# Optimization experiments

Measured on AMD Instinct MI355X. Metric: run time of the kernel, lower is better.

## Reference

```python
import jax, jax.numpy as jnp
import numpy as np

N = 50000    # total nodes in a batched graph
E = 200000   # directed edges (before self loops)
G = 256      # molecules per batch
F_IN = 64    # atom features
H = 4        # gat heads
CH = 128     # hidden_channels (per head)
D = H * CH   # 512, concat width
MLP_H = 128  # hidden_channels * mlp_hidden_factor
NEG_SLOPE = 0.2


def _gat(x, src, dst, W, a_src, a_dst, b, concat):
    """PyG GATConv (eval mode, self loops already added to src/dst)."""
    n = x.shape[0]
    heads, ch = a_src.shape
    h = (x @ W).reshape(n, heads, ch)                       # [N,H,C]
    e = jax.nn.leaky_relu((h * a_src).sum(-1)[src]
                          + (h * a_dst).sum(-1)[dst], NEG_SLOPE)  # [E,H]
    emax = jax.ops.segment_max(e, dst, num_segments=n)
    emax = jnp.where(jnp.isfinite(emax), emax, 0.0)
    p = jnp.exp(e - emax[dst])
    denom = jax.ops.segment_sum(p, dst, num_segments=n)
    alpha = p / (denom[dst] + 1e-16)                        # segment softmax over dst
    out = jax.ops.segment_sum(h[src] * alpha[..., None], dst, num_segments=n)
    out = out.reshape(n, heads * ch) if concat else out.mean(axis=1)
    return out + b


def _encoder(x, edge_index, batch, p):
    n = x.shape[0]
    loop = jnp.arange(n, dtype=edge_index.dtype)            # GATConv add_self_loops=True
    src = jnp.concatenate([edge_index[0], loop])
    dst = jnp.concatenate([edge_index[1], loop])
    x = jax.nn.elu(_gat(x, src, dst, p['W1'], p['as1'], p['ad1'], p['b1'], True))
    x = jax.nn.elu(_gat(x, src, dst, p['W2'], p['as2'], p['ad2'], p['b2'], True))
    x = _gat(x, src, dst, p['W3'], p['as3'], p['ad3'], p['b3'], False)
    emb = jax.ops.segment_max(x, batch, num_segments=G)     # global_max_pool
    return jnp.where(jnp.isfinite(emb), emb, 0.0)


def setup_inputs() -> dict:
    key = jax.random.key(0)
    ks = jax.random.split(key, 24)
    rn = lambda k, s, sc=0.1: jax.random.normal(k, s, jnp.float32) * sc
    return dict(
        x1=rn(ks[0], (N, F_IN), 1.0),
        edge_index1=jax.random.randint(ks[1], (2, E), 0, N, dtype=jnp.int32),
        batch1=jnp.sort(jax.random.randint(ks[2], (N,), 0, G, dtype=jnp.int32)),
        x2=rn(ks[3], (N, F_IN), 1.0),
        edge_index2=jax.random.randint(ks[4], (2, E), 0, N, dtype=jnp.int32),
        batch2=jnp.sort(jax.random.randint(ks[5], (N,), 0, G, dtype=jnp.int32)),
        W1=rn(ks[6], (F_IN, D)), as1=rn(ks[7], (H, CH)), ad1=rn(ks[8], (H, CH)),
        b1=jnp.zeros((D,), jnp.float32),
        W2=rn(ks[9], (D, D)), as2=rn(ks[10], (H, CH)), ad2=rn(ks[11], (H, CH)),
        b2=jnp.zeros((D,), jnp.float32),
        W3=rn(ks[12], (D, CH)), as3=rn(ks[13], (1, CH)), ad3=rn(ks[14], (1, CH)),
        b3=jnp.zeros((CH,), jnp.float32),
        mw1=rn(ks[15], (2 * CH, MLP_H)), mb1=jnp.zeros((MLP_H,), jnp.float32),
        mw2=rn(ks[16], (MLP_H, 1)), mb2=jnp.zeros((1,), jnp.float32),
    )


def reference(x1, edge_index1, batch1, x2, edge_index2, batch2,
              W1, as1, ad1, b1, W2, as2, ad2, b2, W3, as3, ad3, b3,
              mw1, mb1, mw2, mb2):
    p = dict(W1=W1, as1=as1, ad1=ad1, b1=b1,
             W2=W2, as2=as2, ad2=ad2, b2=b2,
             W3=W3, as3=as3, ad3=ad3, b3=b3)
    e1 = _encoder(x1, edge_index1, batch1, p)               # [G, CH]
    e2 = _encoder(x2, edge_index2, batch2, p)               # [G, CH]
    z = jnp.concatenate([e1, e2], axis=-1)                  # [G, 2*CH]
    return jax.nn.relu(z @ mw1 + mb1) @ mw2 + mb2           # [G, 1]
```

## Files before the change

kernel.cpp:

```cpp
#include <hip/hip_runtime.h>
#include <cstdint>

namespace {
constexpr int kN = 50000;
constexpr int kE = 200000;
constexpr int kE2 = kE + kN;
constexpr int kG = 256;
constexpr float kNegSlope = 0.2f;
}

using half8   = __attribute__((ext_vector_type(8))) _Float16;
using floatx4 = __attribute__((ext_vector_type(4))) float;

__device__ __forceinline__ void gld_lds16(const void* g, void* l) {
  __builtin_amdgcn_global_load_lds(
      (const __attribute__((address_space(1))) unsigned int*)g,
      (__attribute__((address_space(3))) unsigned int*)l, 16, 0, 0);
}

__device__ __forceinline__ float fexp(float x) {
  return __builtin_amdgcn_exp2f(x * 1.44269504088896f);
}

template <int OUTF16, int BN, int CT>
__global__ __launch_bounds__(512, 2) void gemm_ring(
    const _Float16* __restrict__ A, const _Float16* __restrict__ B,
    void* __restrict__ Cv, int M, int N, int K) {
  constexpr int ASL = 1024;
  constexpr int BSL = BN * 4;
  constexpr int SLOT = (ASL + BSL) * 16;
  constexpr int LPT = (ASL + BSL) / 512;
  constexpr int WN = (BN == 256) ? 4 : 2;
  constexpr int WM = 8 / WN;
  constexpr int WTM = 256 / WM;
  constexpr int WTN = BN / WN;
  constexpr int MI = WTM / 16;
  constexpr int NI = WTN / 16;
  __shared__ alignas(16) char smem[4 * SLOT];
  const int t = threadIdx.x;
  const int w = t >> 6, l = t & 63;
  const int x = blockIdx.x & 7, s = blockIdx.x >> 3;
  const int col = (CT == 1) ? 0 : (s & (CT - 1));
  const int rt = ((CT == 1) ? s : (s >> 1)) * 8 + x;
  const int bm = rt * 256;
  const int bn = col * BN;
  if (bm >= M) return;
  const int wr = w / WN, wc = w % WN;
  const int quad = l >> 4, lrow = l & 15;

  floatx4 acc[MI][NI];
#pragma unroll
  for (int mi = 0; mi < MI; ++mi)
#pragma unroll
    for (int ni = 0; ni < NI; ++ni) acc[mi][ni] = (floatx4){0.f, 0.f, 0.f, 0.f};

  auto stageA = [&](int kt) {
    char* buf = smem + (size_t)(kt & 3) * SLOT;
    int k0 = kt * 32;
    k0 = (k0 > K - 32) ? (K - 32) : k0;
#pragma unroll
    for (int i = 0; i < 2; ++i) {
      const int sl = i * 512 + t;
      const int row = ((sl >> 6) << 4) + (sl & 15);
      const int q = (sl >> 4) & 3;
      int ga = bm + row;
      ga = (ga < M) ? ga : (M - 1);
      gld_lds16(A + (size_t)ga * K + k0 + q * 8, buf + sl * 16);
    }
  };
  auto stageB = [&](int kt) {
    char* buf = smem + (size_t)(kt & 3) * SLOT + ASL * 16;
    int k0 = kt * 32;
    k0 = (k0 > K - 32) ? (K - 32) : k0;
#pragma unroll
    for (int i = 0; i < LPT - 2; ++i) {
      const int sl = i * 512 + t;
      const int row = ((sl >> 6) << 4) + (sl & 15);
      const int q = (sl >> 4) & 3;
      gld_lds16(B + (size_t)(bn + row) * K + k0 + q * 8, buf + sl * 16);
    }
  };

  stageA(0); stageB(0);
  stageA(1); stageB(1);
  stageA(2); stageB(2);

  const int NT = K >> 5;
  for (int kt = 0; kt < NT; ++kt) {
    char* bufc = smem + (size_t)(kt & 3) * SLOT;
    stageA(kt + 3);
    if constexpr (BN == 256)
      asm volatile("s_waitcnt vmcnt(10)" ::: "memory");
    else
      asm volatile("s_waitcnt vmcnt(8)" ::: "memory");
    __builtin_amdgcn_s_barrier();
    asm volatile("" ::: "memory");
    half8 fa[MI], fb[NI];
#pragma unroll
    for (int ni = 0; ni < NI; ++ni)
      fb[ni] = *(const half8*)(bufc + ASL * 16 + ((wc * NI + ni) << 10) + l * 16);
#pragma unroll
    for (int mi = 0; mi < MI / 2; ++mi)
      fa[mi] = *(const half8*)(bufc + ((wr * MI + mi) << 10) + l * 16);
    __builtin_amdgcn_s_setprio(1);
#pragma unroll
    for (int mi = 0; mi < MI / 2; ++mi)
#pragma unroll
      for (int ni = 0; ni < NI; ++ni)
        acc[mi][ni] = __builtin_amdgcn_mfma_f32_16x16x32_f16(
            fa[mi], fb[ni], acc[mi][ni], 0, 0, 0);
    __builtin_amdgcn_s_setprio(0);
    stageB(kt + 3);
#pragma unroll
    for (int mi = MI / 2; mi < MI; ++mi)
      fa[mi] = *(const half8*)(bufc + ((wr * MI + mi) << 10) + l * 16);
    __builtin_amdgcn_s_setprio(1);
#pragma unroll
    for (int mi = MI / 2; mi < MI; ++mi)
#pragma unroll
      for (int ni = 0; ni < NI; ++ni)
        acc[mi][ni] = __builtin_amdgcn_mfma_f32_16x16x32_f16(
            fa[mi], fb[ni], acc[mi][ni], 0, 0, 0);
    __builtin_amdgcn_s_setprio(0);
    asm volatile("" ::: "memory");
    __builtin_amdgcn_s_barrier();
  }
  asm volatile("s_waitcnt vmcnt(0)" ::: "memory");
  const int colbase = bn + wc * WTN + lrow;
#pragma unroll
  for (int mi = 0; mi < MI; ++mi) {
    const int rbase = bm + wr * WTM + mi * 16 + quad * 4;
#pragma unroll
    for (int r = 0; r < 4; ++r) {
      const int grow = rbase + r;
      if (grow < M) {
        if constexpr (OUTF16) {
          _Float16* C = (_Float16*)Cv;
#pragma unroll
          for (int ni = 0; ni < NI; ++ni)
            C[(size_t)grow * N + colbase + ni * 16] = (_Float16)acc[mi][ni][r];
        } else {
          float* C = (float*)Cv;
#pragma unroll
          for (int ni = 0; ni < NI; ++ni)
            C[(size_t)grow * N + colbase + ni * 16] = acc[mi][ni][r];
        }
      }
    }
  }
}

__global__ void wt_split_all(const float* __restrict__ W1, _Float16* Th1,
                             const float* __restrict__ W2, _Float16* Th2,
                             const float* __restrict__ W3, _Float16* Th3) {
  int idx = blockIdx.x * blockDim.x + threadIdx.x;
  const float* W;
  _Float16* Th;
  int K, N;
  if (idx < 64 * 512) {
    W = W1; Th = Th1; K = 64; N = 512;
  } else if (idx < 64 * 512 + 512 * 512) {
    idx -= 64 * 512;
    W = W2; Th = Th2; K = 512; N = 512;
  } else if (idx < 64 * 512 + 512 * 512 + 512 * 128) {
    idx -= 64 * 512 + 512 * 512;
    W = W3; Th = Th3; K = 512; N = 128;
  } else {
    return;
  }
  const int k = idx / N;
  const int n = idx - k * N;
  Th[n * K + k] = (_Float16)W[idx];
}

__global__ void prep2(const float* __restrict__ x0, const float* __restrict__ x1,
                      _Float16* __restrict__ Xh, int* __restrict__ cnt,
                      int* __restrict__ total) {
  const int idx = blockIdx.x * blockDim.x + threadIdx.x;
  const int half = kN * 64;
  if (idx < half) Xh[idx] = (_Float16)x0[idx];
  else if (idx < 2 * half) Xh[idx] = (_Float16)x1[idx - half];
  if (idx < 2 * kN) cnt[idx] = 1;
  if (idx == 0) *total = 0;
}
__global__ void prep(const float* __restrict__ X, _Float16* __restrict__ Xh,
                     int* __restrict__ cnt, int* __restrict__ total, int nsplit,
                     int n) {
  const int idx = blockIdx.x * blockDim.x + threadIdx.x;
  if (idx < nsplit) Xh[idx] = (_Float16)X[idx];
  if (idx < n) cnt[idx] = 1;
  if (idx == 0) *total = 0;
}

__global__ void count_edges2(const int* __restrict__ d0, const int* __restrict__ d1,
                             int* __restrict__ cnt) {
  const int i = blockIdx.x * blockDim.x + threadIdx.x;
  if (i < kE) atomicAdd(&cnt[d0[i]], 1);
  else if (i < 2 * kE) atomicAdd(&cnt[d1[i - kE] + kN], 1);
}
__global__ void fill_edges2(const int* __restrict__ s0, const int* __restrict__ d0,
                            const int* __restrict__ s1, const int* __restrict__ d1,
                            int* __restrict__ cursor, int* __restrict__ csr) {
  const int i = blockIdx.x * blockDim.x + threadIdx.x;
  if (i < kE) {
    const int p = atomicAdd(&cursor[d0[i]], 1);
    csr[p] = s0[i];
  } else if (i < 2 * kE) {
    const int j = i - kE;
    const int p = atomicAdd(&cursor[d1[j] + kN], 1);
    csr[p] = s1[j] + kN;
  }
}
__global__ void count_edges(const int* __restrict__ dst, int* __restrict__ cnt,
                            int ne) {
  const int i = blockIdx.x * blockDim.x + threadIdx.x;
  if (i < ne) atomicAdd(&cnt[dst[i]], 1);
}
__global__ void fill_edges(const int* __restrict__ src, const int* __restrict__ dst,
                           int* __restrict__ cursor, int* __restrict__ csr, int ne) {
  const int i = blockIdx.x * blockDim.x + threadIdx.x;
  if (i < ne) {
    const int p = atomicAdd(&cursor[dst[i]], 1);
    csr[p] = src[i];
  }
}
__global__ void alloc_ranges(const int* __restrict__ cnt, int* __restrict__ start,
                             int* __restrict__ cursor, int* __restrict__ total,
                             int* __restrict__ csr, int n) {
  const int i = blockIdx.x * blockDim.x + threadIdx.x;
  const int lane = threadIdx.x & 63;
  const int v = (i < n) ? cnt[i] : 0;
  int sc = v;
#pragma unroll
  for (int off = 1; off < 64; off <<= 1) {
    const int t = __shfl_up(sc, off);
    if (lane >= off) sc += t;
  }
  const int wtot = __shfl(sc, 63);
  int base = 0;
  if (lane == 63) base = atomicAdd(total, wtot);
  base = __shfl(base, 63);
  const int st = base + sc - v;
  if (i < n) {
    start[i] = st;
    cursor[i] = st + 1;
    csr[st] = i;
  }
}

__global__ void gat_agg4(const _Float16* __restrict__ h,
                         const float* __restrict__ a_src,
                         const float* __restrict__ a_dst,
                         const int* __restrict__ start, const int* __restrict__ cnt,
                         const int* __restrict__ csr_src,
                         const float* __restrict__ bias,
                         _Float16* __restrict__ outH, int n_nodes) {
  const int gtid = blockIdx.x * blockDim.x + threadIdx.x;
  const int node = gtid >> 6;
  const int lane = threadIdx.x & 63;
  if (node >= n_nodes) return;
  const int ch = lane * 8;
  float as_r[8], ad_r[8];
#pragma unroll
  for (int j = 0; j < 8; ++j) {
    as_r[j] = a_src[ch + j];
    ad_r[j] = a_dst[ch + j];
  }
  const int s = start[node];
  const int c = cnt[node];
  const half8 vs = *(const half8*)(h + (size_t)node * 512 + ch);
  float fs[8];
  float t_src = 0.f, t_dst = 0.f;
#pragma unroll
  for (int j = 0; j < 8; ++j) {
    fs[j] = (float)vs[j];
    t_src = fmaf(fs[j], as_r[j], t_src);
    t_dst = fmaf(fs[j], ad_r[j], t_dst);
  }
#pragma unroll
  for (int off = 1; off < 16; off <<= 1) {
    t_src += __shfl_xor(t_src, off);
    t_dst += __shfl_xor(t_dst, off);
  }
  const float ad = t_dst;
  float es = t_src + ad;
  es = (es > 0.f) ? es : kNegSlope * es;
  const float ws = fexp(es);
  float d0 = ws, d1 = 0.f;
  float a0[8], a1[8];
#pragma unroll
  for (int j = 0; j < 8; ++j) {
    a0[j] = ws * fs[j];
    a1[j] = 0.f;
  }
  int i = 1;
  for (; i + 2 <= c; i += 2) {
    const int s0 = csr_src[s + i];
    const int s1 = csr_src[s + i + 1];
    const half8 v0 = *(const half8*)(h + (size_t)s0 * 512 + ch);
    const half8 v1 = *(const half8*)(h + (size_t)s1 * 512 + ch);
    float f0[8], f1[8];
    float t0 = 0.f, t1 = 0.f;
#pragma unroll
    for (int j = 0; j < 8; ++j) {
      f0[j] = (float)v0[j];
      f1[j] = (float)v1[j];
      t0 = fmaf(f0[j], as_r[j], t0);
      t1 = fmaf(f1[j], as_r[j], t1);
    }
#pragma unroll
    for (int off = 1; off < 16; off <<= 1) {
      t0 += __shfl_xor(t0, off);
      t1 += __shfl_xor(t1, off);
    }
    float e0 = t0 + ad;
    float e1 = t1 + ad;
    e0 = (e0 > 0.f) ? e0 : kNegSlope * e0;
    e1 = (e1 > 0.f) ? e1 : kNegSlope * e1;
    const float w0 = fexp(e0);
    const float w1 = fexp(e1);
    d0 += w0;
    d1 += w1;
#pragma unroll
    for (int j = 0; j < 8; ++j) {
      a0[j] = fmaf(w0, f0[j], a0[j]);
      a1[j] = fmaf(w1, f1[j], a1[j]);
    }
  }
  if (i < c) {
    const int s0 = csr_src[s + i];
    const half8 v0 = *(const half8*)(h + (size_t)s0 * 512 + ch);
    float f0[8];
    float t0 = 0.f;
#pragma unroll
    for (int j = 0; j < 8; ++j) {
      f0[j] = (float)v0[j];
      t0 = fmaf(f0[j], as_r[j], t0);
    }
#pragma unroll
    for (int off = 1; off < 16; off <<= 1) t0 += __shfl_xor(t0, off);
    float e0 = t0 + ad;
    e0 = (e0 > 0.f) ? e0 : kNegSlope * e0;
    const float w0 = fexp(e0);
    d0 += w0;
#pragma unroll
    for (int j = 0; j < 8; ++j) a0[j] = fmaf(w0, f0[j], a0[j]);
  }
  const float inv = 1.f / (d0 + d1 + 1e-16f);
  half8 H;
#pragma unroll
  for (int j = 0; j < 8; ++j) {
    float v = (a0[j] + a1[j]) * inv + bias[ch + j];
    v = (v > 0.f) ? v : (fexp(v) - 1.f);
    H[j] = (_Float16)v;
  }
  *(half8*)(outH + (size_t)node * 512 + ch) = H;
}

__global__ void gat_agg_l3(const float* __restrict__ h,
                           const float* __restrict__ a_src,
                           const float* __restrict__ a_dst,
                           const int* __restrict__ start, const int* __restrict__ cnt,
                           const int* __restrict__ csr_src,
                           const float* __restrict__ bias,
                           float* __restrict__ out, int n_nodes) {
  const int gtid = blockIdx.x * blockDim.x + threadIdx.x;
  const int node = gtid >> 6;
  const int lane = threadIdx.x & 63;
  if (node >= n_nodes) return;
  const float2 asv = *(const float2*)(a_src + lane * 2);
  const float2 adv = *(const float2*)(a_dst + lane * 2);
  const int s = start[node];
  const int c = cnt[node];
  const float2 vs = *(const float2*)(h + (size_t)node * 128 + lane * 2);
  float t_src = fmaf(vs.x, asv.x, vs.y * asv.y);
  float t_dst = fmaf(vs.x, adv.x, vs.y * adv.y);
#pragma unroll
  for (int off = 1; off < 64; off <<= 1) {
    t_src += __shfl_xor(t_src, off);
    t_dst += __shfl_xor(t_dst, off);
  }
  const float ad = t_dst;
  float es = t_src + ad;
  es = (es > 0.f) ? es : kNegSlope * es;
  const float ws = fexp(es);
  float2 a0 = make_float2(ws * vs.x, ws * vs.y);
  float2 a1 = make_float2(0.f, 0.f);
  float d0 = ws, d1 = 0.f;
  int i = 1;
  for (; i + 2 <= c; i += 2) {
    const int s0 = csr_src[s + i];
    const int s1 = csr_src[s + i + 1];
    const float2 v0 = *(const float2*)(h + (size_t)s0 * 128 + lane * 2);
    const float2 v1 = *(const float2*)(h + (size_t)s1 * 128 + lane * 2);
    float t0 = fmaf(v0.x, asv.x, v0.y * asv.y);
    float t1 = fmaf(v1.x, asv.x, v1.y * asv.y);
#pragma unroll
    for (int off = 1; off < 64; off <<= 1) {
      t0 += __shfl_xor(t0, off);
      t1 += __shfl_xor(t1, off);
    }
    float e0 = t0 + ad;
    float e1 = t1 + ad;
    e0 = (e0 > 0.f) ? e0 : kNegSlope * e0;
    e1 = (e1 > 0.f) ? e1 : kNegSlope * e1;
    const float w0 = fexp(e0);
    const float w1 = fexp(e1);
    d0 += w0;
    d1 += w1;
    a0.x = fmaf(w0, v0.x, a0.x); a1.x = fmaf(w1, v1.x, a1.x);
    a0.y = fmaf(w0, v0.y, a0.y); a1.y = fmaf(w1, v1.y, a1.y);
  }
  if (i < c) {
    const int s0 = csr_src[s + i];
    const float2 v0 = *(const float2*)(h + (size_t)s0 * 128 + lane * 2);
    float t0 = fmaf(v0.x, asv.x, v0.y * asv.y);
#pragma unroll
    for (int off = 1; off < 64; off <<= 1) t0 += __shfl_xor(t0, off);
    float e0 = t0 + ad;
    e0 = (e0 > 0.f) ? e0 : kNegSlope * e0;
    const float w0 = fexp(e0);
    d0 += w0;
    a0.x = fmaf(w0, v0.x, a0.x);
    a0.y = fmaf(w0, v0.y, a0.y);
  }
  const float inv = 1.f / (d0 + d1 + 1e-16f);
  *(float2*)(out + (size_t)node * 128 + lane * 2) =
      make_float2((a0.x + a1.x) * inv + bias[lane * 2],
                  (a0.y + a1.y) * inv + bias[lane * 2 + 1]);
}

__global__ void pool_max2(const float* __restrict__ x, const int* __restrict__ bt1,
                          const int* __restrict__ bt2, float* __restrict__ emb) {
  __shared__ int lohi[2];
  const int enc = blockIdx.x >> 8;
  const int g = blockIdx.x & 255;
  const int* batch = enc ? bt2 : bt1;
  const float* xx = x + (size_t)enc * kN * 128;
  if (threadIdx.x == 0) {
    int lo = 0, hi = kN;
    while (lo < hi) {
      const int mid = (lo + hi) >> 1;
      if (batch[mid] < g) lo = mid + 1; else hi = mid;
    }
    lohi[0] = lo;
    hi = kN;
    while (lo < hi) {
      const int mid = (lo + hi) >> 1;
      if (batch[mid] < g + 1) lo = mid + 1; else hi = mid;
    }
    lohi[1] = lo;
  }
  __syncthreads();
  const int lo = lohi[0], hi = lohi[1];
  const int c = threadIdx.x;
  float m = -1e30f;
  for (int nid = lo; nid < hi; ++nid) m = fmaxf(m, xx[(size_t)nid * 128 + c]);
  emb[(size_t)blockIdx.x * 128 + c] = (lo < hi) ? m : 0.f;
}
__global__ void pool_max(const float* __restrict__ x, const int* __restrict__ batch,
                         float* __restrict__ emb, int n_nodes) {
  __shared__ int lohi[2];
  const int g = blockIdx.x;
  if (threadIdx.x == 0) {
    int lo = 0, hi = n_nodes;
    while (lo < hi) {
      const int mid = (lo + hi) >> 1;
      if (batch[mid] < g) lo = mid + 1; else hi = mid;
    }
    lohi[0] = lo;
    hi = n_nodes;
    while (lo < hi) {
      const int mid = (lo + hi) >> 1;
      if (batch[mid] < g + 1) lo = mid + 1; else hi = mid;
    }
    lohi[1] = lo;
  }
  __syncthreads();
  const int lo = lohi[0], hi = lohi[1];
  const int c = threadIdx.x;
  float m = -1e30f;
  for (int nid = lo; nid < hi; ++nid) m = fmaxf(m, x[(size_t)nid * 128 + c]);
  emb[g * 128 + c] = (lo < hi) ? m : 0.f;
}

__global__ void mlp_head(const float* __restrict__ e1, const float* __restrict__ e2,
                         const float* __restrict__ mw1, const float* __restrict__ mb1,
                         const float* __restrict__ mw2, const float* __restrict__ mb2,
                         float* __restrict__ out) {
  __shared__ float z[256];
  __shared__ float red[128];
  const int g = blockIdx.x;
  const int j = threadIdx.x;
  z[j] = e1[g * 128 + j];
  z[j + 128] = e2[g * 128 + j];
  __syncthreads();
  float acc = mb1[j];
  for (int k = 0; k < 256; ++k) acc = fmaf(z[k], mw1[k * 128 + j], acc);
  acc = fmaxf(acc, 0.f) * mw2[j];
  red[j] = acc;
  __syncthreads();
  for (int s = 64; s > 0; s >>= 1) {
    if (j < s) red[j] += red[j + s];
    __syncthreads();
  }
  if (j == 0) out[g] = red[0] + mb2[0];
}

namespace {
struct Bufs {
  _Float16 *R1h, *R2h;
  float *R1f, *R2f, *asrc, *adst;
  int *cnt, *start, *cursor, *csr, *total;
  _Float16 *Wth1, *Wth2, *Wth3;
  float* emb;
  size_t need;
};

Bufs plan(void* d_ws, int M, int E) {
  Bufs b;
  char* w = (char*)d_ws;
  size_t off = 0;
  auto take = [&](size_t bytes) -> void* {
    void* p = w + off;
    off += (bytes + 255) & ~(size_t)255;
    return p;
  };
  b.R1h = (_Float16*)take((size_t)M * 512 * 2);
  b.R1f = (float*)b.R1h;
  b.R2h = (_Float16*)take((size_t)M * 512 * 2);
  b.R2f = (float*)b.R2h;
  b.asrc = (float*)take((size_t)M * 4 * 4);
  b.adst = (float*)take((size_t)M * 4 * 4);
  b.cnt = (int*)take((size_t)M * 4);
  b.start = (int*)take((size_t)M * 4);
  b.cursor = (int*)take((size_t)M * 4);
  b.csr = (int*)take((size_t)E * 4);
  b.total = (int*)take(256);
  b.Wth1 = (_Float16*)take((size_t)64 * 512 * 2);
  b.Wth2 = (_Float16*)take((size_t)512 * 512 * 2);
  b.Wth3 = (_Float16*)take((size_t)512 * 128 * 2);
  b.emb = (float*)take((size_t)2 * kG * 128 * 4);
  b.need = off;
  return b;
}

void run_layers(const Bufs& b, void* const* d_in, int M, hipStream_t stream) {
  const float* as1 = (const float*)d_in[7];
  const float* ad1 = (const float*)d_in[8];
  const float* b1 = (const float*)d_in[9];
  const float* as2 = (const float*)d_in[11];
  const float* ad2 = (const float*)d_in[12];
  const float* b2 = (const float*)d_in[13];
  const float* as3 = (const float*)d_in[15];
  const float* ad3 = (const float*)d_in[16];
  const float* b3 = (const float*)d_in[17];
  const int nodeBlocks = (M * 64) / 256;
  const int MT = (M + 255) / 256;
  const int SP = (MT + 7) / 8;

  gemm_ring<1, 256, 2><<<SP * 16, 512, 0, stream>>>(b.R1h, b.Wth1, b.R2h, M, 512, 64);
  gat_agg4<<<nodeBlocks, 256, 0, stream>>>(b.R2h, as1, ad1, b.start, b.cnt,
                                           b.csr, b1, b.R1h, M);
  gemm_ring<1, 256, 2><<<SP * 16, 512, 0, stream>>>(b.R1h, b.Wth2, b.R2h, M, 512, 512);
  gat_agg4<<<nodeBlocks, 256, 0, stream>>>(b.R2h, as2, ad2, b.start, b.cnt,
                                           b.csr, b2, b.R1h, M);
  gemm_ring<0, 128, 1><<<SP * 8, 512, 0, stream>>>(b.R1h, b.Wth3, b.R2f, M, 128, 512);
  gat_agg_l3<<<nodeBlocks, 256, 0, stream>>>(b.R2f, as3, ad3, b.start, b.cnt,
                                             b.csr, b3, b.R1f, M);
}
}

extern "C" void kernel_launch(void* const* d_in, const int* in_sizes, int n_in,
                              void* d_out, int out_size, void* d_ws, size_t ws_size,
                              hipStream_t stream) {
  (void)in_sizes; (void)n_in; (void)out_size;
  const float* W1 = (const float*)d_in[6];
  const float* W2 = (const float*)d_in[10];
  const float* W3 = (const float*)d_in[14];
  const float* mw1 = (const float*)d_in[18];
  const float* mb1 = (const float*)d_in[19];
  const float* mw2 = (const float*)d_in[20];
  const float* mb2 = (const float*)d_in[21];

  Bufs bc = plan(d_ws, 2 * kN, 2 * kE2);
  const bool combined = bc.need <= ws_size;
  Bufs b = combined ? bc : plan(d_ws, kN, kE2);

  const int wtot = 64 * 512 + 512 * 512 + 512 * 128;
  wt_split_all<<<(wtot + 255) / 256, 256, 0, stream>>>(W1, b.Wth1, W2, b.Wth2, W3,
                                                       b.Wth3);
  if (combined) {
    const int M = 2 * kN;
    const int* ei0 = (const int*)d_in[1];
    const int* ei1 = (const int*)d_in[4];
    prep2<<<(2 * kN * 64 + 255) / 256, 256, 0, stream>>>(
        (const float*)d_in[0], (const float*)d_in[3], b.R1h, b.cnt, b.total);
    count_edges2<<<(2 * kE + 255) / 256, 256, 0, stream>>>(ei0 + kE, ei1 + kE,
                                                           b.cnt);
    alloc_ranges<<<(M + 255) / 256, 256, 0, stream>>>(b.cnt, b.start, b.cursor,
                                                      b.total, b.csr, M);
    fill_edges2<<<(2 * kE + 255) / 256, 256, 0, stream>>>(ei0, ei0 + kE, ei1,
                                                          ei1 + kE, b.cursor, b.csr);
    run_layers(b, d_in, M, stream);
    pool_max2<<<2 * kG, 128, 0, stream>>>(b.R1f, (const int*)d_in[2],
                                          (const int*)d_in[5], b.emb);
  } else {
    for (int enc = 0; enc < 2; ++enc) {
      const float* x = (const float*)d_in[enc * 3 + 0];
      const int* ei = (const int*)d_in[enc * 3 + 1];
      const int* batch = (const int*)d_in[enc * 3 + 2];
      prep<<<(kN * 64 + 255) / 256, 256, 0, stream>>>(x, b.R1h, b.cnt, b.total,
                                                      kN * 64, kN);
      count_edges<<<(kE + 255) / 256, 256, 0, stream>>>(ei + kE, b.cnt, kE);
      alloc_ranges<<<(kN + 255) / 256, 256, 0, stream>>>(b.cnt, b.start, b.cursor,
                                                         b.total, b.csr, kN);
      fill_edges<<<(kE + 255) / 256, 256, 0, stream>>>(ei, ei + kE, b.cursor, b.csr,
                                                       kE);
      run_layers(b, d_in, kN, stream);
      pool_max<<<kG, 128, 0, stream>>>(b.R1f, batch, b.emb + (size_t)enc * kG * 128,
                                       kN);
    }
  }
  mlp_head<<<kG, 128, 0, stream>>>(b.emb, b.emb + (size_t)kG * 128, mw1, mb1, mw2,
                                   mb2, (float*)d_out);
}
```

Measured before the change: 671.9 us.

## Fuse per-node attention logit computation into GEMM epilogue

The GEMM epilogue now computes per-node, per-head source and destination attention dot products from the fp32 accumulators and accumulates them with atomics into a zero-initialised buffer. The aggregation kernels then read these precomputed scalars instead of recomputing the dot products and 16/64-lane shuffle reductions for every edge. Self-loop handling moves into the regular CSR loop. The cost is extra atomics and shuffles in the GEMM epilogue, plus an extra buffer that must be cleared in prep. The logits also come from fp32 accumulators rather than fp16-rounded values, which changes numerics slightly.

```diff
diff --git a/kernel.cpp b/kernel.cpp
--- a/kernel.cpp
+++ b/kernel.cpp
@@ -22,10 +22,12 @@
   return __builtin_amdgcn_exp2f(x * 1.44269504088896f);
 }
 
-template <int OUTF16, int BN, int CT>
+template <int OUTF16, int BN, int CT, int HEADS>
 __global__ __launch_bounds__(512, 2) void gemm_ring(
     const _Float16* __restrict__ A, const _Float16* __restrict__ B,
-    void* __restrict__ Cv, int M, int N, int K) {
+    void* __restrict__ Cv, const float* __restrict__ av_src,
+    const float* __restrict__ av_dst, float* __restrict__ aS,
+    float* __restrict__ aD, int M, int N, int K) {
   constexpr int ASL = 1024;
   constexpr int BSL = BN * 4;
   constexpr int SLOT = (ASL + BSL) * 16;
@@ -127,6 +129,15 @@
   }
   asm volatile("s_waitcnt vmcnt(0)" ::: "memory");
   const int colbase = bn + wc * WTN + lrow;
+  float asc[NI], adc[NI];
+  if constexpr (HEADS > 0) {
+#pragma unroll
+    for (int ni = 0; ni < NI; ++ni) {
+      asc[ni] = av_src[colbase + ni * 16];
+      adc[ni] = av_dst[colbase + ni * 16];
+    }
+  }
+  const int head = (HEADS > 1) ? ((bn + wc * WTN) >> 7) : 0;
 #pragma unroll
   for (int mi = 0; mi < MI; ++mi) {
     const int rbase = bm + wr * WTM + mi * 16 + quad * 4;
@@ -144,6 +155,23 @@
 #pragma unroll
           for (int ni = 0; ni < NI; ++ni)
             C[(size_t)grow * N + colbase + ni * 16] = acc[mi][ni][r];
+        }
+      }
+      if constexpr (HEADS > 0) {
+        float ps = 0.f, pd = 0.f;
+#pragma unroll
+        for (int ni = 0; ni < NI; ++ni) {
+          ps = fmaf(acc[mi][ni][r], asc[ni], ps);
+          pd = fmaf(acc[mi][ni][r], adc[ni], pd);
+        }
+#pragma unroll
+        for (int off = 1; off < 16; off <<= 1) {
+          ps += __shfl_xor(ps, off);
+          pd += __shfl_xor(pd, off);
+        }
+        if (lrow == 0 && grow < M) {
+          atomicAdd(aS + (size_t)grow * HEADS + head, ps);
+          atomicAdd(aD + (size_t)grow * HEADS + head, pd);
         }
       }
     }
@@ -175,20 +203,23 @@
 
 __global__ void prep2(const float* __restrict__ x0, const float* __restrict__ x1,
                       _Float16* __restrict__ Xh, int* __restrict__ cnt,
-                      int* __restrict__ total) {
+                      int* __restrict__ total, float* __restrict__ alpha,
+                      int an) {
   const int idx = blockIdx.x * blockDim.x + threadIdx.x;
   const int half = kN * 64;
   if (idx < half) Xh[idx] = (_Float16)x0[idx];
   else if (idx < 2 * half) Xh[idx] = (_Float16)x1[idx - half];
   if (idx < 2 * kN) cnt[idx] = 1;
+  if (idx < an) alpha[idx] = 0.f;
   if (idx == 0) *total = 0;
 }
 __global__ void prep(const float* __restrict__ X, _Float16* __restrict__ Xh,
                      int* __restrict__ cnt, int* __restrict__ total, int nsplit,
-                     int n) {
+                     int n, float* __restrict__ alpha, int an) {
   const int idx = blockIdx.x * blockDim.x + threadIdx.x;
   if (idx < nsplit) Xh[idx] = (_Float16)X[idx];
   if (idx < n) cnt[idx] = 1;
+  if (idx < an) alpha[idx] = 0.f;
   if (idx == 0) *total = 0;
 }
 
@@ -249,8 +280,8 @@
 }
 
 __global__ void gat_agg4(const _Float16* __restrict__ h,
-                         const float* __restrict__ a_src,
-                         const float* __restrict__ a_dst,
+                         const float* __restrict__ asrc,
+                         const float* __restrict__ adst,
                          const int* __restrict__ start, const int* __restrict__ cnt,
                          const int* __restrict__ csr_src,
                          const float* __restrict__ bias,
@@ -260,91 +291,43 @@
   const int lane = threadIdx.x & 63;
   if (node >= n_nodes) return;
   const int ch = lane * 8;
-  float as_r[8], ad_r[8];
-#pragma unroll
-  for (int j = 0; j < 8; ++j) {
-    as_r[j] = a_src[ch + j];
-    ad_r[j] = a_dst[ch + j];
-  }
+  const int head = lane >> 4;
   const int s = start[node];
   const int c = cnt[node];
-  const half8 vs = *(const half8*)(h + (size_t)node * 512 + ch);
-  float fs[8];
-  float t_src = 0.f, t_dst = 0.f;
-#pragma unroll
-  for (int j = 0; j < 8; ++j) {
-    fs[j] = (float)vs[j];
-    t_src = fmaf(fs[j], as_r[j], t_src);
-    t_dst = fmaf(fs[j], ad_r[j], t_dst);
-  }
-#pragma unroll
-  for (int off = 1; off < 16; off <<= 1) {
-    t_src += __shfl_xor(t_src, off);
-    t_dst += __shfl_xor(t_dst, off);
-  }
-  const float ad = t_dst;
-  float es = t_src + ad;
-  es = (es > 0.f) ? es : kNegSlope * es;
-  const float ws = fexp(es);
-  float d0 = ws, d1 = 0.f;
+  const float ad = adst[node * 4 + head];
+  float d0 = 0.f, d1 = 0.f;
   float a0[8], a1[8];
 #pragma unroll
-  for (int j = 0; j < 8; ++j) {
-    a0[j] = ws * fs[j];
-    a1[j] = 0.f;
-  }
-  int i = 1;
+  for (int j = 0; j < 8; ++j) { a0[j] = 0.f; a1[j] = 0.f; }
+  int i = 0;
   for (; i + 2 <= c; i += 2) {
     const int s0 = csr_src[s + i];
     const int s1 = csr_src[s + i + 1];
-    const half8 v0 = *(const half8*)(h + (size_t)s0 * 512 + ch);
-    const half8 v1 = *(const half8*)(h + (size_t)s1 * 512 + ch);
-    float f0[8], f1[8];
-    float t0 = 0.f, t1 = 0.f;
-#pragma unroll
-    for (int j = 0; j < 8; ++j) {
-      f0[j] = (float)v0[j];
-      f1[j] = (float)v1[j];
-      t0 = fmaf(f0[j], as_r[j], t0);
-      t1 = fmaf(f1[j], as_r[j], t1);
-    }
-#pragma unroll
-    for (int off = 1; off < 16; off <<= 1) {
-      t0 += __shfl_xor(t0, off);
-      t1 += __shfl_xor(t1, off);
-    }
-    float e0 = t0 + ad;
-    float e1 = t1 + ad;
+    float e0 = asrc[s0 * 4 + head] + ad;
+    float e1 = asrc[s1 * 4 + head] + ad;
     e0 = (e0 > 0.f) ? e0 : kNegSlope * e0;
     e1 = (e1 > 0.f) ? e1 : kNegSlope * e1;
     const float w0 = fexp(e0);
     const float w1 = fexp(e1);
+    const half8 v0 = *(const half8*)(h + (size_t)s0 * 512 + ch);
+    const half8 v1 = *(const half8*)(h + (size_t)s1 * 512 + ch);
     d0 += w0;
     d1 += w1;
 #pragma unroll
     for (int j = 0; j < 8; ++j) {
-      a0[j] = fmaf(w0, f0[j], a0[j]);
-      a1[j] = fmaf(w1, f1[j], a1[j]);
+      a0[j] = fmaf(w0, (float)v0[j], a0[j]);
+      a1[j] = fmaf(w1, (float)v1[j], a1[j]);
     }
   }
   if (i < c) {
     const int s0 = csr_src[s + i];
-    const half8 v0 = *(const half8*)(h + (size_t)s0 * 512 + ch);
-    float f0[8];
-    float t0 = 0.f;
-#pragma unroll
-    for (int j = 0; j < 8; ++j) {
-      f0[j] = (float)v0[j];
-      t0 = fmaf(f0[j], as_r[j], t0);
-    }
-#pragma unroll
-    for (int off = 1; off < 16; off <<= 1) t0 += __shfl_xor(t0, off);
-    float e0 = t0 + ad;
+    float e0 = asrc[s0 * 4 + head] + ad;
     e0 = (e0 > 0.f) ? e0 : kNegSlope * e0;
     const float w0 = fexp(e0);
+    const half8 v0 = *(const half8*)(h + (size_t)s0 * 512 + ch);
     d0 += w0;
 #pragma unroll
-    for (int j = 0; j < 8; ++j) a0[j] = fmaf(w0, f0[j], a0[j]);
+    for (int j = 0; j < 8; ++j) a0[j] = fmaf(w0, (float)v0[j], a0[j]);
   }
   const float inv = 1.f / (d0 + d1 + 1e-16f);
   half8 H;
@@ -358,8 +341,8 @@
 }
 
 __global__ void gat_agg_l3(const float* __restrict__ h,
-                           const float* __restrict__ a_src,
-                           const float* __restrict__ a_dst,
+                           const float* __restrict__ asrc,
+                           const float* __restrict__ adst,
                            const int* __restrict__ start, const int* __restrict__ cnt,
                            const int* __restrict__ csr_src,
                            const float* __restrict__ bias,
@@ -368,44 +351,24 @@
   const int node = gtid >> 6;
   const int lane = threadIdx.x & 63;
   if (node >= n_nodes) return;
-  const float2 asv = *(const float2*)(a_src + lane * 2);
-  const float2 adv = *(const float2*)(a_dst + lane * 2);
   const int s = start[node];
   const int c = cnt[node];
-  const float2 vs = *(const float2*)(h + (size_t)node * 128 + lane * 2);
-  float t_src = fmaf(vs.x, asv.x, vs.y * asv.y);
-  float t_dst = fmaf(vs.x, adv.x, vs.y * adv.y);
-#pragma unroll
-  for (int off = 1; off < 64; off <<= 1) {
-    t_src += __shfl_xor(t_src, off);
-    t_dst += __shfl_xor(t_dst, off);
-  }
-  const float ad = t_dst;
-  float es = t_src + ad;
-  es = (es > 0.f) ? es : kNegSlope * es;
-  const float ws = fexp(es);
-  float2 a0 = make_float2(ws * vs.x, ws * vs.y);
+  const float ad = adst[node];
+  float2 a0 = make_float2(0.f, 0.f);
   float2 a1 = make_float2(0.f, 0.f);
-  float d0 = ws, d1 = 0.f;
-  int i = 1;
+  float d0 = 0.f, d1 = 0.f;
+  int i = 0;
   for (; i + 2 <= c; i += 2) {
     const int s0 = csr_src[s + i];
     const int s1 = csr_src[s + i + 1];
-    const float2 v0 = *(const float2*)(h + (size_t)s0 * 128 + lane * 2);
-    const float2 v1 = *(const float2*)(h + (size_t)s1 * 128 + lane * 2);
-    float t0 = fmaf(v0.x, asv.x, v0.y * asv.y);
-    float t1 = fmaf(v1.x, asv.x, v1.y * asv.y);
-#pragma unroll
-    for (int off = 1; off < 64; off <<= 1) {
-      t0 += __shfl_xor(t0, off);
-      t1 += __shfl_xor(t1, off);
-    }
-    float e0 = t0 + ad;
-    float e1 = t1 + ad;
+    float e0 = asrc[s0] + ad;
+    float e1 = asrc[s1] + ad;
     e0 = (e0 > 0.f) ? e0 : kNegSlope * e0;
     e1 = (e1 > 0.f) ? e1 : kNegSlope * e1;
     const float w0 = fexp(e0);
     const float w1 = fexp(e1);
+    const float2 v0 = *(const float2*)(h + (size_t)s0 * 128 + lane * 2);
+    const float2 v1 = *(const float2*)(h + (size_t)s1 * 128 + lane * 2);
     d0 += w0;
     d1 += w1;
     a0.x = fmaf(w0, v0.x, a0.x); a1.x = fmaf(w1, v1.x, a1.x);
@@ -413,13 +376,10 @@
   }
   if (i < c) {
     const int s0 = csr_src[s + i];
-    const float2 v0 = *(const float2*)(h + (size_t)s0 * 128 + lane * 2);
-    float t0 = fmaf(v0.x, asv.x, v0.y * asv.y);
-#pragma unroll
-    for (int off = 1; off < 64; off <<= 1) t0 += __shfl_xor(t0, off);
-    float e0 = t0 + ad;
+    float e0 = asrc[s0] + ad;
     e0 = (e0 > 0.f) ? e0 : kNegSlope * e0;
     const float w0 = fexp(e0);
+    const float2 v0 = *(const float2*)(h + (size_t)s0 * 128 + lane * 2);
     d0 += w0;
     a0.x = fmaf(w0, v0.x, a0.x);
     a0.y = fmaf(w0, v0.y, a0.y);
@@ -510,7 +470,8 @@
 namespace {
 struct Bufs {
   _Float16 *R1h, *R2h;
-  float *R1f, *R2f, *asrc, *adst;
+  float *R1f, *R2f;
+  float *alpha;
   int *cnt, *start, *cursor, *csr, *total;
   _Float16 *Wth1, *Wth2, *Wth3;
   float* emb;
@@ -530,8 +491,7 @@
   b.R1f = (float*)b.R1h;
   b.R2h = (_Float16*)take((size_t)M * 512 * 2);
   b.R2f = (float*)b.R2h;
-  b.asrc = (float*)take((size_t)M * 4 * 4);
-  b.adst = (float*)take((size_t)M * 4 * 4);
+  b.alpha = (float*)take((size_t)M * 18 * 4);
   b.cnt = (int*)take((size_t)M * 4);
   b.start = (int*)take((size_t)M * 4);
   b.cursor = (int*)take((size_t)M * 4);
@@ -555,18 +515,27 @@
   const float* as3 = (const float*)d_in[15];
   const float* ad3 = (const float*)d_in[16];
   const float* b3 = (const float*)d_in[17];
+  float* aS1 = b.alpha;
+  float* aD1 = b.alpha + (size_t)M * 4;
+  float* aS2 = b.alpha + (size_t)M * 8;
+  float* aD2 = b.alpha + (size_t)M * 12;
+  float* aS3 = b.alpha + (size_t)M * 16;
+  float* aD3 = b.alpha + (size_t)M * 17;
   const int nodeBlocks = (M * 64) / 256;
   const int MT = (M + 255) / 256;
   const int SP = (MT + 7) / 8;
 
-  gemm_ring<1, 256, 2><<<SP * 16, 512, 0, stream>>>(b.R1h, b.Wth1, b.R2h, M, 512, 64);
-  gat_agg4<<<nodeBlocks, 256, 0, stream>>>(b.R2h, as1, ad1, b.start, b.cnt,
+  gemm_ring<1, 256, 2, 4><<<SP * 16, 512, 0, stream>>>(
+      b.R1h, b.Wth1, b.R2h, as1, ad1, aS1, aD1, M, 512, 64);
+  gat_agg4<<<nodeBlocks, 256, 0, stream>>>(b.R2h, aS1, aD1, b.start, b.cnt,
                                            b.csr, b1, b.R1h, M);
-  gemm_ring<1, 256, 2><<<SP * 16, 512, 0, stream>>>(b.R1h, b.Wth2, b.R2h, M, 512, 512);
-  gat_agg4<<<nodeBlocks, 256, 0, stream>>>(b.R2h, as2, ad2, b.start, b.cnt,
+  gemm_ring<1, 256, 2, 4><<<SP * 16, 512, 0, stream>>>(
+      b.R1h, b.Wth2, b.R2h, as2, ad2, aS2, aD2, M, 512, 512);
+  gat_agg4<<<nodeBlocks, 256, 0, stream>>>(b.R2h, aS2, aD2, b.start, b.cnt,
                                            b.csr, b2, b.R1h, M);
-  gemm_ring<0, 128, 1><<<SP * 8, 512, 0, stream>>>(b.R1h, b.Wth3, b.R2f, M, 128, 512);
-  gat_agg_l3<<<nodeBlocks, 256, 0, stream>>>(b.R2f, as3, ad3, b.start, b.cnt,
+  gemm_ring<0, 128, 1, 1><<<SP * 8, 512, 0, stream>>>(
+      b.R1h, b.Wth3, b.R2f, as3, ad3, aS3, aD3, M, 128, 512);
+  gat_agg_l3<<<nodeBlocks, 256, 0, stream>>>(b.R2f, aS3, aD3, b.start, b.cnt,
                                              b.csr, b3, b.R1f, M);
 }
 }
@@ -595,7 +564,8 @@
     const int* ei0 = (const int*)d_in[1];
     const int* ei1 = (const int*)d_in[4];
     prep2<<<(2 * kN * 64 + 255) / 256, 256, 0, stream>>>(
-        (const float*)d_in[0], (const float*)d_in[3], b.R1h, b.cnt, b.total);
+        (const float*)d_in[0], (const float*)d_in[3], b.R1h, b.cnt, b.total,
+        b.alpha, M * 18);
     count_edges2<<<(2 * kE + 255) / 256, 256, 0, stream>>>(ei0 + kE, ei1 + kE,
                                                            b.cnt);
     alloc_ranges<<<(M + 255) / 256, 256, 0, stream>>>(b.cnt, b.start, b.cursor,
@@ -611,7 +581,8 @@
       const int* ei = (const int*)d_in[enc * 3 + 1];
       const int* batch = (const int*)d_in[enc * 3 + 2];
       prep<<<(kN * 64 + 255) / 256, 256, 0, stream>>>(x, b.R1h, b.cnt, b.total,
-                                                      kN * 64, kN);
+                                                      kN * 64, kN, b.alpha,
+                                                      kN * 18);
       count_edges<<<(kE + 255) / 256, 256, 0, stream>>>(ei + kE, b.cnt, kE);
       alloc_ranges<<<(kN + 255) / 256, 256, 0, stream>>>(b.cnt, b.start, b.cursor,
                                                          b.total, b.csr, kN);
```

Result: slower. 815.9 us (+21.4%).
